# Optimization experiments

Measured on AMD Instinct MI355X. Metric: run time of the kernel, lower is better.

Reference implementation:

```python
import jax, jax.numpy as jnp
import numpy as np

EPS = 1e-5

def _layernorm(x, g, b):
    mu = jnp.mean(x, axis=-1, keepdims=True)
    var = jnp.mean(jnp.square(x - mu), axis=-1, keepdims=True)
    return (x - mu) * jax.lax.rsqrt(var + EPS) * g + b

def setup_inputs() -> dict:
    key = jax.random.key(0)
    ks = jax.random.split(key, 12)
    B, S, D, F = 2, 2048, 1024, 4096
    w = lambda k, shp: jax.random.normal(k, shp, dtype=jnp.float32) * 0.02
    return {
        "x":  jax.random.normal(ks[0], (B, S, D), dtype=jnp.float32),
        "Wq": w(ks[1], (D, D)), "bq": jnp.zeros((D,), jnp.float32),
        "Wk": w(ks[2], (D, D)), "bk": jnp.zeros((D,), jnp.float32),
        "Wv": w(ks[3], (D, D)), "bv": jnp.zeros((D,), jnp.float32),
        "W1": w(ks[4], (F, D)), "b1": jnp.zeros((F,), jnp.float32),
        "W2": w(ks[5], (D, F)), "b2": jnp.zeros((D,), jnp.float32),
        "g1": jnp.ones((D,), jnp.float32), "beta1": jnp.zeros((D,), jnp.float32),
        "g2": jnp.ones((D,), jnp.float32), "beta2": jnp.zeros((D,), jnp.float32),
    }

def reference(x, Wq, bq, Wk, bk, Wv, bv, W1, b1, W2, b2, g1, beta1, g2, beta2):
    B, S, D = x.shape
    H = 16
    dk = D // H
    # QKV projections (torch nn.Linear: y = x @ W.T + b)
    q = (x @ Wq.T + bq).reshape(B, S, H, dk).transpose(0, 2, 1, 3)  # [B,H,S,dk]
    k = (x @ Wk.T + bk).reshape(B, S, H, dk).transpose(0, 2, 1, 3)
    v = (x @ Wv.T + bv).reshape(B, S, H, dk).transpose(0, 2, 1, 3)
    # naive full attention (no mask, dropout=identity in eval)
    scores = jnp.einsum("bhqd,bhkd->bhqk", q, k) / jnp.sqrt(jnp.float32(dk))
    probs = jax.nn.softmax(scores, axis=-1)
    attn = jnp.einsum("bhqk,bhkd->bhqd", probs, v)  # [B,H,S,dk]
    attn_out = attn.transpose(0, 2, 1, 3).reshape(B, S, D)  # NOTE: no output proj (combine unused in source)
    # residual + LN1
    h = _layernorm(x + attn_out, g1, beta1)
    # FFN: linear2(relu(linear1(h)))
    ffn = jax.nn.relu(h @ W1.T + b1) @ W2.T + b2
    # residual + LN2
    return _layernorm(h + ffn, g2, beta2)
```

## Files before the change

kernel.cpp:

```cpp
#include <hip/hip_runtime.h>
#include <stdint.h>

typedef unsigned short u16;
typedef __bf16 bf16x8 __attribute__((ext_vector_type(8)));
typedef short s16x8 __attribute__((ext_vector_type(8)));
typedef float f32x4 __attribute__((ext_vector_type(4)));

union FragU { s16x8 s; bf16x8 b; uint4 u; };

__device__ __forceinline__ f32x4 mfma_bf16(s16x8 a, s16x8 b, f32x4 c) {
    FragU ua, ub; ua.s = a; ub.s = b;
    return __builtin_amdgcn_mfma_f32_16x16x32_bf16(ua.b, ub.b, c, 0, 0, 0);
}

__device__ __forceinline__ u16 f2bf(float f) {
    uint32_t u = __float_as_uint(f);
    u += 0x7fffu + ((u >> 16) & 1u);
    return (u16)(u >> 16);
}

__device__ __forceinline__ float bf2f(u16 u) {
    return __uint_as_float((uint32_t)u << 16);
}

__device__ __forceinline__ void gload_lds16(const void* g, void* l) {
    __builtin_amdgcn_global_load_lds((__attribute__((address_space(1))) void*)g,
                                     (__attribute__((address_space(3))) void*)l,
                                     16, 0, 0);
}

__device__ __forceinline__ void xcd_swz(int& bx, int& by, int& bz) {
    int nx = gridDim.x, ny = gridDim.y;
    int nwg = nx * ny * gridDim.z;
    int lin = blockIdx.x + nx * (blockIdx.y + ny * blockIdx.z);
    int cpx = nwg >> 3;
    int s = (lin & 7) * cpx + (lin >> 3);
    bx = s % nx; s /= nx;
    by = s % ny; bz = s / ny;
}

__global__ void k_cast(const float* __restrict__ in, u16* __restrict__ out, int n4) {
    int i = blockIdx.x * blockDim.x + threadIdx.x;
    int stride = gridDim.x * blockDim.x;
    for (; i < n4; i += stride) {
        float4 v = ((const float4*)in)[i];
        u16 us[4] = {f2bf(v.x), f2bf(v.y), f2bf(v.z), f2bf(v.w)};
        *(uint2*)(out + (size_t)i * 4) = *(uint2*)us;
    }
}

template<int RELU, int OUTMODE>
__device__ __forceinline__ void gemm_body(
    const u16* __restrict__ A, const u16* __restrict__ W,
    const float* __restrict__ bias, void* __restrict__ Cout,
    int M, int N, int K, int row0, int col0, int kbeg, int kend)
{
    __shared__ __align__(16) u16 As[128 * 32];
    __shared__ __align__(16) u16 Bs[128 * 32];

    const int tid  = threadIdx.x;
    const int wid  = tid >> 6;
    const int lane = tid & 63;
    const int g    = lane >> 4;
    const int cc   = lane & 15;
    const int wr   = wid >> 1;
    const int wc   = wid & 1;

    f32x4 zero = {0.f, 0.f, 0.f, 0.f};
    f32x4 acc[4][4];
#pragma unroll
    for (int i = 0; i < 4; i++)
#pragma unroll
        for (int j = 0; j < 4; j++) acc[i][j] = zero;

    const int srow = lane >> 2;
    const int scol = (lane & 3) * 8;
    const u16* gA0 = A + (size_t)(row0 + wid * 32 + srow) * K + scol;
    const u16* gB0 = W + (size_t)(col0 + wid * 32 + srow) * K + scol;
    u16* lA0 = &As[(wid * 32) * 32];
    u16* lB0 = &Bs[(wid * 32) * 32];

    for (int k0 = kbeg; k0 < kend; k0 += 32) {
        gload_lds16(gA0 + k0,                  lA0);
        gload_lds16(gA0 + (size_t)16 * K + k0, lA0 + 16 * 32);
        gload_lds16(gB0 + k0,                  lB0);
        gload_lds16(gB0 + (size_t)16 * K + k0, lB0 + 16 * 32);
        __syncthreads();

        s16x8 af[4], bf[4];
#pragma unroll
        for (int mi = 0; mi < 4; mi++)
            af[mi] = *(const s16x8*)&As[(wr * 64 + mi * 16 + cc) * 32 + g * 8];
#pragma unroll
        for (int ni = 0; ni < 4; ni++)
            bf[ni] = *(const s16x8*)&Bs[(wc * 64 + ni * 16 + cc) * 32 + g * 8];
#pragma unroll
        for (int mi = 0; mi < 4; mi++)
#pragma unroll
            for (int ni = 0; ni < 4; ni++)
                acc[mi][ni] = mfma_bf16(af[mi], bf[ni], acc[mi][ni]);
        __syncthreads();
    }

#pragma unroll
    for (int ni = 0; ni < 4; ni++) {
        int col = col0 + wc * 64 + ni * 16 + cc;
        float bvv = 0.f;
        if (OUTMODE != 2) bvv = bias[col];
#pragma unroll
        for (int mi = 0; mi < 4; mi++) {
            int row = row0 + wr * 64 + mi * 16 + g * 4;
#pragma unroll
            for (int r = 0; r < 4; r++) {
                float v = acc[mi][ni][r] + bvv;
                if (RELU) v = fmaxf(v, 0.f);
                size_t idx = (size_t)(row + r) * N + col;
                if (OUTMODE == 0) ((float*)Cout)[idx] = v;
                else              ((u16*)Cout)[idx] = f2bf(v);
            }
        }
    }
}

__global__ __launch_bounds__(256, 4) void k_gemm_qkv(
    const u16* __restrict__ A, const u16* __restrict__ Wq, const u16* __restrict__ Wk,
    const u16* __restrict__ Wv, const float* __restrict__ bq, const float* __restrict__ bk,
    const float* __restrict__ bv, u16* __restrict__ Q, u16* __restrict__ K,
    u16* __restrict__ V, int M, int N, int Kd)
{
    int bx, by, bz; xcd_swz(bx, by, bz);
    const u16* W; const float* bb; u16* out;
    if (bz == 0)      { W = Wq; bb = bq; out = Q; }
    else if (bz == 1) { W = Wk; bb = bk; out = K; }
    else              { W = Wv; bb = bv; out = V; }
    gemm_body<0, 1>(A, W, bb, out, M, N, Kd, by * 128, bx * 128, 0, Kd);
}

__global__ __launch_bounds__(256, 4) void k_gemm_relu_bf16(
    const u16* __restrict__ A, const u16* __restrict__ W, const float* __restrict__ bias,
    u16* __restrict__ C, int M, int N, int K)
{
    int bx, by, bz; xcd_swz(bx, by, bz);
    gemm_body<1, 1>(A, W, bias, C, M, N, K, by * 128, bx * 128, 0, K);
}

__global__ __launch_bounds__(256, 4) void k_gemm_part(
    const u16* __restrict__ A, const u16* __restrict__ W,
    u16* __restrict__ p0, u16* __restrict__ p1, u16* __restrict__ p2, u16* __restrict__ p3,
    int M, int N, int K)
{
    int bx, by, bz; xcd_swz(bx, by, bz);
    u16* out = (bz == 0) ? p0 : (bz == 1) ? p1 : (bz == 2) ? p2 : p3;
    gemm_body<0, 2>(A, W, nullptr, out, M, N, K, by * 128, bx * 128, bz * 1024, bz * 1024 + 1024);
}

__global__ __launch_bounds__(256) void k_transpose_v(const u16* __restrict__ V, u16* __restrict__ Vt)
{
    constexpr int S = 2048, Dm = 1024;
    __shared__ __align__(16) u16 tile[64][72];
    int s0 = blockIdx.x * 64;
    int h = blockIdx.y, b = blockIdx.z;
    int tid = threadIdx.x;
    int r = tid >> 2, ch = tid & 3;
    const u16* src = V + (size_t)(b * S + s0 + r) * Dm + h * 64;
    *(s16x8*)&tile[r][ch * 8]      = *(const s16x8*)(src + ch * 8);
    *(s16x8*)&tile[r][ch * 8 + 32] = *(const s16x8*)(src + ch * 8 + 32);
    __syncthreads();
    int dd = tid >> 2, kc = tid & 3;
    u16 tmp[16];
#pragma unroll
    for (int j = 0; j < 16; j++) tmp[j] = tile[kc * 16 + j][dd];
    u16* dst = Vt + ((size_t)(b * 16 + h) * 64 + dd) * S + s0 + kc * 16;
    *(s16x8*)dst       = *(const s16x8*)&tmp[0];
    *(s16x8*)(dst + 8) = *(const s16x8*)&tmp[8];
}

__global__ __launch_bounds__(512) void k_flash(
    const u16* __restrict__ Q, const u16* __restrict__ Kb,
    const u16* __restrict__ Vt, float* __restrict__ O)
{
    constexpr int S = 2048, Dm = 1024, H = 16;
    constexpr float sc = 0.125f;
    int qt = blockIdx.x, h = blockIdx.y, b = blockIdx.z;
    int tid = threadIdx.x, wid = tid >> 6, lane = tid & 63;
    int g = lane >> 4, cc = lane & 15;

    __shared__ __align__(16) u16 Ks[64 * 72];
    __shared__ __align__(16) u16 Vs[64 * 72];

    int q0 = qt * 128 + wid * 16;
    size_t base = (size_t)b * S * Dm + h * 64;

    FragU uq0, uq1, qs0, qs1;
    uq0.s = *(const s16x8*)(Q + base + (size_t)(q0 + cc) * Dm + g * 8);
    uq1.s = *(const s16x8*)(Q + base + (size_t)(q0 + cc) * Dm + 32 + g * 8);
#pragma unroll
    for (int e = 0; e < 8; e++) {
        qs0.b[e] = (__bf16)((float)uq0.b[e] * sc);
        qs1.b[e] = (__bf16)((float)uq1.b[e] * sc);
    }
    s16x8 qf0 = qs0.s, qf1 = qs1.s;

    f32x4 zero = {0.f, 0.f, 0.f, 0.f};
    f32x4 o[4];
#pragma unroll
    for (int t = 0; t < 4; t++) o[t] = zero;
    float m_run = -1e30f, l_run = 0.f;

    const int sr  = tid >> 3;
    const int sch = (tid & 7) * 8;
    const int colb = 32 * (sch / 32) + 4 * ((sch / 16) & 1) + 8 * ((sch & 15) / 4);
    const u16* kSrc = Kb + base + (size_t)sr * Dm + sch;
    const u16* vSrc = Vt + (size_t)(b * H + h) * 64 * S + (size_t)sr * S + sch;
    u16* kDst  = &Ks[sr * 72 + sch];
    u16* vDst0 = &Vs[sr * 72 + colb];

    s16x8 kpre = *(const s16x8*)kSrc;
    s16x8 vpre = *(const s16x8*)vSrc;

    for (int kv0 = 0; kv0 < S; kv0 += 64) {
        __syncthreads();
        *(s16x8*)kDst = kpre;
        {
            FragU vv; vv.s = vpre;
            *(uint2*)vDst0       = make_uint2(vv.u.x, vv.u.y);
            *(uint2*)(vDst0 + 8) = make_uint2(vv.u.z, vv.u.w);
        }
        __syncthreads();
        if (kv0 + 64 < S) {
            kpre = *(const s16x8*)(kSrc + (size_t)(kv0 + 64) * Dm);
            vpre = *(const s16x8*)(vSrc + (kv0 + 64));
        }

        f32x4 sacc[4];
#pragma unroll
        for (int t = 0; t < 4; t++) sacc[t] = zero;
        __builtin_amdgcn_s_setprio(1);
#pragma unroll
        for (int t = 0; t < 4; t++) {
            s16x8 kf0 = *(const s16x8*)&Ks[(t * 16 + cc) * 72 + g * 8];
            s16x8 kf1 = *(const s16x8*)&Ks[(t * 16 + cc) * 72 + 32 + g * 8];
            sacc[t] = mfma_bf16(kf0, qf0, sacc[t]);
            sacc[t] = mfma_bf16(kf1, qf1, sacc[t]);
        }
        __builtin_amdgcn_s_setprio(0);

        float mx = fmaxf(fmaxf(sacc[0][0], sacc[0][1]), fmaxf(sacc[0][2], sacc[0][3]));
#pragma unroll
        for (int t = 1; t < 4; t++)
            mx = fmaxf(mx, fmaxf(fmaxf(sacc[t][0], sacc[t][1]), fmaxf(sacc[t][2], sacc[t][3])));
        mx = fmaxf(mx, __shfl_xor(mx, 16, 64));
        mx = fmaxf(mx, __shfl_xor(mx, 32, 64));
        float mnew = fmaxf(m_run, mx);
        float a = __expf(m_run - mnew);

        float ssum = 0.f;
        FragU pb[2];
#pragma unroll
        for (int t = 0; t < 4; t++)
#pragma unroll
            for (int r = 0; r < 4; r++) {
                float pv = __expf(sacc[t][r] - mnew);
                ssum += pv;
                pb[t >> 1].b[(t & 1) * 4 + r] = (__bf16)pv;
            }
        ssum += __shfl_xor(ssum, 16, 64);
        ssum += __shfl_xor(ssum, 32, 64);
        l_run = l_run * a + ssum;
        m_run = mnew;
#pragma unroll
        for (int t = 0; t < 4; t++)
#pragma unroll
            for (int i = 0; i < 4; i++) o[t][i] *= a;

        __builtin_amdgcn_s_setprio(1);
#pragma unroll
        for (int td = 0; td < 4; td++) {
            s16x8 vf0 = *(const s16x8*)&Vs[(td * 16 + cc) * 72 + g * 8];
            s16x8 vf1 = *(const s16x8*)&Vs[(td * 16 + cc) * 72 + 32 + g * 8];
            o[td] = mfma_bf16(vf0, pb[0].s, o[td]);
            o[td] = mfma_bf16(vf1, pb[1].s, o[td]);
        }
        __builtin_amdgcn_s_setprio(0);
    }

    float inv = 1.f / l_run;
#pragma unroll
    for (int td = 0; td < 4; td++) {
        float4 st = {o[td][0] * inv, o[td][1] * inv, o[td][2] * inv, o[td][3] * inv};
        *(float4*)&O[(size_t)(b * S + q0 + cc) * Dm + h * 64 + td * 16 + g * 4] = st;
    }
}

template<int WRITE_BF>
__global__ __launch_bounds__(256) void k_ln(
    const float* __restrict__ A, const float* __restrict__ B,
    const float* __restrict__ gw, const float* __restrict__ bw,
    float* __restrict__ outf, u16* __restrict__ outb)
{
    constexpr int D = 1024;
    int row = blockIdx.x;
    int t = threadIdx.x;
    int lane = t & 63, wid = t >> 6;
    float4 va = ((const float4*)(A + (size_t)row * D))[t];
    float4 vb = ((const float4*)(B + (size_t)row * D))[t];
    float v0 = va.x + vb.x, v1 = va.y + vb.y, v2 = va.z + vb.z, v3 = va.w + vb.w;
    float sum = v0 + v1 + v2 + v3;
    float sq  = v0 * v0 + v1 * v1 + v2 * v2 + v3 * v3;
#pragma unroll
    for (int off = 1; off < 64; off <<= 1) {
        sum += __shfl_xor(sum, off, 64);
        sq  += __shfl_xor(sq,  off, 64);
    }
    __shared__ float s1[4], s2[4];
    if (lane == 0) { s1[wid] = sum; s2[wid] = sq; }
    __syncthreads();
    sum = s1[0] + s1[1] + s1[2] + s1[3];
    sq  = s2[0] + s2[1] + s2[2] + s2[3];
    float mu  = sum * (1.f / D);
    float var = sq * (1.f / D) - mu * mu;
    float rs  = rsqrtf(var + 1e-5f);
    float4 gv = ((const float4*)gw)[t];
    float4 bv = ((const float4*)bw)[t];
    float y0 = (v0 - mu) * rs * gv.x + bv.x;
    float y1 = (v1 - mu) * rs * gv.y + bv.y;
    float y2 = (v2 - mu) * rs * gv.z + bv.z;
    float y3 = (v3 - mu) * rs * gv.w + bv.w;
    float4 yo = {y0, y1, y2, y3};
    ((float4*)(outf + (size_t)row * D))[t] = yo;
    if (WRITE_BF) {
        u16 us[4] = {f2bf(y0), f2bf(y1), f2bf(y2), f2bf(y3)};
        *(uint2*)(outb + (size_t)row * D + t * 4) = *(uint2*)us;
    }
}

__global__ __launch_bounds__(256) void k_ln2(
    const float* __restrict__ A,
    const u16* __restrict__ p0, const u16* __restrict__ p1,
    const u16* __restrict__ p2, const u16* __restrict__ p3,
    const float* __restrict__ bias,
    const float* __restrict__ gw, const float* __restrict__ bw,
    float* __restrict__ outf)
{
    constexpr int D = 1024;
    int row = blockIdx.x;
    int t = threadIdx.x;
    int lane = t & 63, wid = t >> 6;
    size_t idx = (size_t)row * D + t * 4;
    float4 va = ((const float4*)(A + (size_t)row * D))[t];
    float4 bb = ((const float4*)bias)[t];
    float v0 = va.x + bb.x, v1 = va.y + bb.y, v2 = va.z + bb.z, v3 = va.w + bb.w;
    const u16* ps[4] = {p0, p1, p2, p3};
#pragma unroll
    for (int pi = 0; pi < 4; pi++) {
        uint2 q = *(const uint2*)(ps[pi] + idx);
        v0 += bf2f((u16)q.x);
        v1 += bf2f((u16)(q.x >> 16));
        v2 += bf2f((u16)q.y);
        v3 += bf2f((u16)(q.y >> 16));
    }
    float sum = v0 + v1 + v2 + v3;
    float sq  = v0 * v0 + v1 * v1 + v2 * v2 + v3 * v3;
#pragma unroll
    for (int off = 1; off < 64; off <<= 1) {
        sum += __shfl_xor(sum, off, 64);
        sq  += __shfl_xor(sq,  off, 64);
    }
    __shared__ float s1[4], s2[4];
    if (lane == 0) { s1[wid] = sum; s2[wid] = sq; }
    __syncthreads();
    sum = s1[0] + s1[1] + s1[2] + s1[3];
    sq  = s2[0] + s2[1] + s2[2] + s2[3];
    float mu  = sum * (1.f / D);
    float var = sq * (1.f / D) - mu * mu;
    float rs  = rsqrtf(var + 1e-5f);
    float4 gv = ((const float4*)gw)[t];
    float4 bv = ((const float4*)bw)[t];
    float4 yo = {(v0 - mu) * rs * gv.x + bv.x,
                 (v1 - mu) * rs * gv.y + bv.y,
                 (v2 - mu) * rs * gv.z + bv.z,
                 (v3 - mu) * rs * gv.w + bv.w};
    ((float4*)(outf + (size_t)row * D))[t] = yo;
}

extern "C" void kernel_launch(void* const* d_in, const int* in_sizes, int n_in,
                              void* d_out, int out_size, void* d_ws, size_t ws_size,
                              hipStream_t stream)
{
    constexpr int B = 2, S = 2048, D = 1024, F = 4096, H = 16;
    constexpr int M = B * S;
    const float* x   = (const float*)d_in[0];
    const float* Wq  = (const float*)d_in[1];
    const float* bq  = (const float*)d_in[2];
    const float* Wk  = (const float*)d_in[3];
    const float* bk  = (const float*)d_in[4];
    const float* Wv  = (const float*)d_in[5];
    const float* bv  = (const float*)d_in[6];
    const float* W1  = (const float*)d_in[7];
    const float* b1  = (const float*)d_in[8];
    const float* W2  = (const float*)d_in[9];
    const float* b2  = (const float*)d_in[10];
    const float* g1  = (const float*)d_in[11];
    const float* be1 = (const float*)d_in[12];
    const float* g2  = (const float*)d_in[13];
    const float* be2 = (const float*)d_in[14];
    float* out = (float*)d_out;

    char* ws = (char*)d_ws;
    size_t off = 0;
    auto alloc = [&](size_t bytes) {
        void* p = ws + off;
        off += (bytes + 255) & ~(size_t)255;
        return p;
    };
    u16* xb   = (u16*)alloc((size_t)M * D * 2);
    u16* wqb  = (u16*)alloc((size_t)D * D * 2);
    u16* wkb  = (u16*)alloc((size_t)D * D * 2);
    u16* wvb  = (u16*)alloc((size_t)D * D * 2);
    u16* w1b  = (u16*)alloc((size_t)F * D * 2);
    u16* w2b  = (u16*)alloc((size_t)D * F * 2);
    u16* Qb   = (u16*)alloc((size_t)M * D * 2);
    u16* Kbf  = (u16*)alloc((size_t)M * D * 2);
    u16* Vb   = (u16*)alloc((size_t)M * D * 2);
    u16* Vtb  = (u16*)alloc((size_t)M * D * 2);
    float* attn = (float*)alloc((size_t)M * D * 4);
    float* hf   = (float*)alloc((size_t)M * D * 4);
    u16* hb     = (u16*)alloc((size_t)M * D * 2);
    u16* ffn1   = Qb;
    u16* p0 = xb;
    u16* p1 = w1b;
    u16* p2 = (u16*)attn;
    u16* p3 = ((u16*)attn) + (size_t)M * D;

    dim3 blk(256);
    k_cast<<<dim3(512), blk, 0, stream>>>(x,  xb,  M * D / 4);
    k_cast<<<dim3(256), blk, 0, stream>>>(Wq, wqb, D * D / 4);
    k_cast<<<dim3(256), blk, 0, stream>>>(Wk, wkb, D * D / 4);
    k_cast<<<dim3(256), blk, 0, stream>>>(Wv, wvb, D * D / 4);
    k_cast<<<dim3(512), blk, 0, stream>>>(W1, w1b, F * D / 4);
    k_cast<<<dim3(512), blk, 0, stream>>>(W2, w2b, D * F / 4);

    k_gemm_qkv<<<dim3(D / 128, M / 128, 3), blk, 0, stream>>>(
        xb, wqb, wkb, wvb, bq, bk, bv, Qb, Kbf, Vb, M, D, D);
    k_transpose_v<<<dim3(S / 64, H, B), blk, 0, stream>>>(Vb, Vtb);
    k_flash<<<dim3(S / 128, H, B), dim3(512), 0, stream>>>(Qb, Kbf, Vtb, attn);
    k_ln<1><<<dim3(M), blk, 0, stream>>>(x, attn, g1, be1, hf, hb);
    k_gemm_relu_bf16<<<dim3(F / 128, M / 128), blk, 0, stream>>>(hb, w1b, b1, ffn1, M, F, D);
    k_gemm_part<<<dim3(D / 128, M / 128, 4), blk, 0, stream>>>(
        ffn1, w2b, p0, p1, p2, p3, M, D, F);
    k_ln2<<<dim3(M), blk, 0, stream>>>(hf, p0, p1, p2, p3, b2, g2, be2, out);
}
```

Measured before the change: 229.2 us.

## Double K-step in GEMM with swizzled LDS, widen flash KV tile and lazy rescale

The GEMM now stages 64-wide K slices per iteration with an XOR-swizzled LDS layout. This halves the barriers per K and avoids bank conflicts from the wider rows. The flash attention kernel processes 128 keys per iteration and loads K directly to LDS with swizzling. It also skips the online-softmax rescale unless the running max grows by more than a threshold. These cut barriers, LDS conflicts and exp/multiply work, at the cost of more LDS per block and possible occupancy loss.

```diff
diff --git a/kernel.cpp b/kernel.cpp
--- a/kernel.cpp
+++ b/kernel.cpp
@@ -55,8 +55,8 @@
     const float* __restrict__ bias, void* __restrict__ Cout,
     int M, int N, int K, int row0, int col0, int kbeg, int kend)
 {
-    __shared__ __align__(16) u16 As[128 * 32];
-    __shared__ __align__(16) u16 Bs[128 * 32];
+    __shared__ __align__(16) u16 As[128 * 64];
+    __shared__ __align__(16) u16 Bs[128 * 64];
 
     const int tid  = threadIdx.x;
     const int wid  = tid >> 6;
@@ -73,32 +73,40 @@
 #pragma unroll
         for (int j = 0; j < 4; j++) acc[i][j] = zero;
 
-    const int srow = lane >> 2;
-    const int scol = (lane & 3) * 8;
-    const u16* gA0 = A + (size_t)(row0 + wid * 32 + srow) * K + scol;
-    const u16* gB0 = W + (size_t)(col0 + wid * 32 + srow) * K + scol;
-    u16* lA0 = &As[(wid * 32) * 32];
-    u16* lB0 = &Bs[(wid * 32) * 32];
-
-    for (int k0 = kbeg; k0 < kend; k0 += 32) {
-        gload_lds16(gA0 + k0,                  lA0);
-        gload_lds16(gA0 + (size_t)16 * K + k0, lA0 + 16 * 32);
-        gload_lds16(gB0 + k0,                  lB0);
-        gload_lds16(gB0 + (size_t)16 * K + k0, lB0 + 16 * 32);
+    const int srow = tid >> 3;
+    const int scol = ((tid & 7) ^ (srow & 7)) * 8;
+    const u16* gA0 = A + (size_t)(row0 + srow) * K + scol;
+    const u16* gB0 = W + (size_t)(col0 + srow) * K + scol;
+    u16* lA0 = &As[wid * 512];
+    u16* lB0 = &Bs[wid * 512];
+
+    const int xm = (cc & 7);
+
+    for (int k0 = kbeg; k0 < kend; k0 += 64) {
+#pragma unroll
+        for (int j = 0; j < 4; j++)
+            gload_lds16(gA0 + (size_t)(j * 32) * K + k0, lA0 + j * 2048);
+#pragma unroll
+        for (int j = 0; j < 4; j++)
+            gload_lds16(gB0 + (size_t)(j * 32) * K + k0, lB0 + j * 2048);
         __syncthreads();
 
-        s16x8 af[4], bf[4];
-#pragma unroll
-        for (int mi = 0; mi < 4; mi++)
-            af[mi] = *(const s16x8*)&As[(wr * 64 + mi * 16 + cc) * 32 + g * 8];
-#pragma unroll
-        for (int ni = 0; ni < 4; ni++)
-            bf[ni] = *(const s16x8*)&Bs[(wc * 64 + ni * 16 + cc) * 32 + g * 8];
-#pragma unroll
-        for (int mi = 0; mi < 4; mi++)
+#pragma unroll
+        for (int h = 0; h < 2; h++) {
+            const int slot = ((h * 4 + g) ^ xm) * 8;
+            s16x8 af[4], bf[4];
+#pragma unroll
+            for (int mi = 0; mi < 4; mi++)
+                af[mi] = *(const s16x8*)&As[(wr * 64 + mi * 16 + cc) * 64 + slot];
 #pragma unroll
             for (int ni = 0; ni < 4; ni++)
-                acc[mi][ni] = mfma_bf16(af[mi], bf[ni], acc[mi][ni]);
+                bf[ni] = *(const s16x8*)&Bs[(wc * 64 + ni * 16 + cc) * 64 + slot];
+#pragma unroll
+            for (int mi = 0; mi < 4; mi++)
+#pragma unroll
+                for (int ni = 0; ni < 4; ni++)
+                    acc[mi][ni] = mfma_bf16(af[mi], bf[ni], acc[mi][ni]);
+        }
         __syncthreads();
     }
 
@@ -175,18 +183,19 @@
     *(s16x8*)(dst + 8) = *(const s16x8*)&tmp[8];
 }
 
-__global__ __launch_bounds__(512) void k_flash(
+__global__ __launch_bounds__(512, 4) void k_flash(
     const u16* __restrict__ Q, const u16* __restrict__ Kb,
     const u16* __restrict__ Vt, float* __restrict__ O)
 {
     constexpr int S = 2048, Dm = 1024, H = 16;
+    constexpr int KVB = 128;
     constexpr float sc = 0.125f;
     int qt = blockIdx.x, h = blockIdx.y, b = blockIdx.z;
     int tid = threadIdx.x, wid = tid >> 6, lane = tid & 63;
     int g = lane >> 4, cc = lane & 15;
 
-    __shared__ __align__(16) u16 Ks[64 * 72];
-    __shared__ __align__(16) u16 Vs[64 * 72];
+    __shared__ __align__(16) u16 Ks[128 * 64];
+    __shared__ __align__(16) u16 Vs[64 * 128];
 
     int q0 = qt * 128 + wid * 16;
     size_t base = (size_t)b * S * Dm + h * 64;
@@ -207,39 +216,54 @@
     for (int t = 0; t < 4; t++) o[t] = zero;
     float m_run = -1e30f, l_run = 0.f;
 
-    const int sr  = tid >> 3;
-    const int sch = (tid & 7) * 8;
-    const int colb = 32 * (sch / 32) + 4 * ((sch / 16) & 1) + 8 * ((sch & 15) / 4);
-    const u16* kSrc = Kb + base + (size_t)sr * Dm + sch;
-    const u16* vSrc = Vt + (size_t)(b * H + h) * 64 * S + (size_t)sr * S + sch;
-    u16* kDst  = &Ks[sr * 72 + sch];
-    u16* vDst0 = &Vs[sr * 72 + colb];
-
-    s16x8 kpre = *(const s16x8*)kSrc;
-    s16x8 vpre = *(const s16x8*)vSrc;
-
-    for (int kv0 = 0; kv0 < S; kv0 += 64) {
+    const int krow = tid >> 3;
+    const int kcol = ((tid & 7) ^ (krow & 7)) * 8;
+    const u16* kSrcBase = Kb + base + (size_t)krow * Dm + kcol;
+    u16* kDst0 = &Ks[wid * 512];
+    u16* kDst1 = kDst0 + 4096;
+
+    const int vrow = tid >> 3;
+    const int vch  = (tid & 7) * 8;
+    const int xmv  = (vrow & 7) << 3;
+    const int cb0  = ((vch >> 5) << 5) | (((vch >> 4) & 1) << 2) | (((vch >> 2) & 3) << 3);
+    const int cb1  = cb0 + 64;
+    const u16* vSrcBase = Vt + (size_t)(b * H + h) * 64 * S + (size_t)vrow * S;
+    u16* vq0a = &Vs[(vrow * 128 + cb0) ^ xmv];
+    u16* vq0b = &Vs[(vrow * 128 + cb0 + 8) ^ xmv];
+    u16* vq1a = &Vs[(vrow * 128 + cb1) ^ xmv];
+    u16* vq1b = &Vs[(vrow * 128 + cb1 + 8) ^ xmv];
+
+    s16x8 vpre0 = *(const s16x8*)(vSrcBase + vch);
+    s16x8 vpre1 = *(const s16x8*)(vSrcBase + 64 + vch);
+
+    const int xm = cc & 7;
+
+    for (int kv0 = 0; kv0 < S; kv0 += KVB) {
         __syncthreads();
-        *(s16x8*)kDst = kpre;
+        gload_lds16(kSrcBase + (size_t)kv0 * Dm,        kDst0);
+        gload_lds16(kSrcBase + (size_t)(kv0 + 64) * Dm, kDst1);
         {
-            FragU vv; vv.s = vpre;
-            *(uint2*)vDst0       = make_uint2(vv.u.x, vv.u.y);
-            *(uint2*)(vDst0 + 8) = make_uint2(vv.u.z, vv.u.w);
+            FragU a0, a1; a0.s = vpre0; a1.s = vpre1;
+            *(uint2*)vq0a = make_uint2(a0.u.x, a0.u.y);
+            *(uint2*)vq0b = make_uint2(a0.u.z, a0.u.w);
+            *(uint2*)vq1a = make_uint2(a1.u.x, a1.u.y);
+            *(uint2*)vq1b = make_uint2(a1.u.z, a1.u.w);
         }
         __syncthreads();
-        if (kv0 + 64 < S) {
-            kpre = *(const s16x8*)(kSrc + (size_t)(kv0 + 64) * Dm);
-            vpre = *(const s16x8*)(vSrc + (kv0 + 64));
-        }
-
-        f32x4 sacc[4];
-#pragma unroll
-        for (int t = 0; t < 4; t++) sacc[t] = zero;
+        if (kv0 + KVB < S) {
+            vpre0 = *(const s16x8*)(vSrcBase + kv0 + KVB + vch);
+            vpre1 = *(const s16x8*)(vSrcBase + kv0 + KVB + 64 + vch);
+        }
+
+        f32x4 sacc[8];
+#pragma unroll
+        for (int t = 0; t < 8; t++) sacc[t] = zero;
         __builtin_amdgcn_s_setprio(1);
 #pragma unroll
-        for (int t = 0; t < 4; t++) {
-            s16x8 kf0 = *(const s16x8*)&Ks[(t * 16 + cc) * 72 + g * 8];
-            s16x8 kf1 = *(const s16x8*)&Ks[(t * 16 + cc) * 72 + 32 + g * 8];
+        for (int t = 0; t < 8; t++) {
+            const u16* kr = &Ks[(t * 16 + cc) * 64];
+            s16x8 kf0 = *(const s16x8*)(kr + ((0 + g) ^ xm) * 8);
+            s16x8 kf1 = *(const s16x8*)(kr + ((4 + g) ^ xm) * 8);
             sacc[t] = mfma_bf16(kf0, qf0, sacc[t]);
             sacc[t] = mfma_bf16(kf1, qf1, sacc[t]);
         }
@@ -247,39 +271,45 @@
 
         float mx = fmaxf(fmaxf(sacc[0][0], sacc[0][1]), fmaxf(sacc[0][2], sacc[0][3]));
 #pragma unroll
-        for (int t = 1; t < 4; t++)
+        for (int t = 1; t < 8; t++)
             mx = fmaxf(mx, fmaxf(fmaxf(sacc[t][0], sacc[t][1]), fmaxf(sacc[t][2], sacc[t][3])));
         mx = fmaxf(mx, __shfl_xor(mx, 16, 64));
         mx = fmaxf(mx, __shfl_xor(mx, 32, 64));
-        float mnew = fmaxf(m_run, mx);
-        float a = __expf(m_run - mnew);
+
+        if (!__all(mx - m_run <= 8.f)) {
+            float mnew = fmaxf(m_run, mx);
+            float a = __expf(m_run - mnew);
+            l_run *= a;
+#pragma unroll
+            for (int t = 0; t < 4; t++)
+#pragma unroll
+                for (int i = 0; i < 4; i++) o[t][i] *= a;
+            m_run = mnew;
+        }
 
         float ssum = 0.f;
-        FragU pb[2];
-#pragma unroll
-        for (int t = 0; t < 4; t++)
+        FragU pb[4];
+#pragma unroll
+        for (int t = 0; t < 8; t++)
 #pragma unroll
             for (int r = 0; r < 4; r++) {
-                float pv = __expf(sacc[t][r] - mnew);
+                float pv = __expf(sacc[t][r] - m_run);
                 ssum += pv;
                 pb[t >> 1].b[(t & 1) * 4 + r] = (__bf16)pv;
             }
         ssum += __shfl_xor(ssum, 16, 64);
         ssum += __shfl_xor(ssum, 32, 64);
-        l_run = l_run * a + ssum;
-        m_run = mnew;
-#pragma unroll
-        for (int t = 0; t < 4; t++)
-#pragma unroll
-            for (int i = 0; i < 4; i++) o[t][i] *= a;
+        l_run += ssum;
 
         __builtin_amdgcn_s_setprio(1);
 #pragma unroll
         for (int td = 0; td < 4; td++) {
-            s16x8 vf0 = *(const s16x8*)&Vs[(td * 16 + cc) * 72 + g * 8];
-            s16x8 vf1 = *(const s16x8*)&Vs[(td * 16 + cc) * 72 + 32 + g * 8];
-            o[td] = mfma_bf16(vf0, pb[0].s, o[td]);
-            o[td] = mfma_bf16(vf1, pb[1].s, o[td]);
+            const int rb = (td * 16 + cc) * 128;
+#pragma unroll
+            for (int kk = 0; kk < 4; kk++) {
+                s16x8 vf = *(const s16x8*)&Vs[(rb + kk * 32 + g * 8) ^ (xm << 3)];
+                o[td] = mfma_bf16(vf, pb[kk].s, o[td]);
+            }
         }
         __builtin_amdgcn_s_setprio(0);
     }
```

Measured after the change: 213.7 us. -6.8%, faster.
